# Performance work log

Hardware: AMD Instinct MI355X
Metric: run time of the kernel (lower is better)

## Reference

```python
import jax, jax.numpy as jnp
import numpy as np

NEG_SLOPE = 0.2  # PyG GATConv default negative_slope
EPS = 1e-16      # PyG softmax denominator eps


def gat_layer(x, src, dst, W, b, a_src, a_dst, n_nodes):
    # x: [N, Fin]; W: [Fout, Fin]; a_src/a_dst: [Fout] (heads=1, concat)
    h = x @ W.T                                   # [N, Fout]
    al_s = h @ a_src                              # [N]
    al_d = h @ a_dst                              # [N]
    e = jax.nn.leaky_relu(al_s[src] + al_d[dst], NEG_SLOPE)   # [E]
    m = jax.lax.stop_gradient(
        jax.ops.segment_max(e, dst, num_segments=n_nodes))   # stable softmax per target
    ex = jnp.exp(e - m[dst])
    denom = jax.ops.segment_sum(ex, dst, num_segments=n_nodes)
    alpha = ex / (denom[dst] + EPS)               # [E]
    out = jax.ops.segment_sum(alpha[:, None] * h[src], dst, num_segments=n_nodes)
    return out + b


def reference(x, edge_index, W0, b0, asrc0, adst0, W1, b1, asrc1, adst1):
    B, N, _ = x.shape
    # GATConv adds self-loops by default
    loops = jnp.arange(N, dtype=edge_index.dtype)
    src = jnp.concatenate([edge_index[0], loops])
    dst = jnp.concatenate([edge_index[1], loops])

    def per_graph(xb):
        h = jax.nn.relu(gat_layer(xb, src, dst, W0, b0, asrc0, adst0, N))
        h = jax.nn.relu(gat_layer(h, src, dst, W1, b1, asrc1, adst1, N))
        return h

    return jax.vmap(per_graph)(x)  # [B, N, Fout]


def setup_inputs() -> dict:
    key = jax.random.key(0)
    ks = jax.random.split(key, 10)
    B, N, E = 4, 10000, 320000
    F0, F1, F2 = 256, 256, 128
    x = jax.random.normal(ks[0], (B, N, F0), dtype=jnp.float32)
    edge_index = jax.random.randint(ks[1], (2, E), 0, N, dtype=jnp.int64)
    s0 = 1.0 / np.sqrt(F0)
    s1 = 1.0 / np.sqrt(F1)
    return {
        "x": x,
        "edge_index": edge_index,
        "W0": jax.random.normal(ks[2], (F1, F0), dtype=jnp.float32) * s0,
        "b0": jnp.zeros((F1,), dtype=jnp.float32),
        "asrc0": jax.random.normal(ks[3], (F1,), dtype=jnp.float32) * s1,
        "adst0": jax.random.normal(ks[4], (F1,), dtype=jnp.float32) * s1,
        "W1": jax.random.normal(ks[5], (F2, F1), dtype=jnp.float32) * s1,
        "b1": jnp.zeros((F2,), dtype=jnp.float32),
        "asrc1": jax.random.normal(ks[6], (F2,), dtype=jnp.float32) / np.sqrt(F2),
        "adst1": jax.random.normal(ks[7], (F2,), dtype=jnp.float32) / np.sqrt(F2),
    }
```

## Files before the change

kernel.cpp:

```cpp
#include <hip/hip_runtime.h>
#include <hip/hip_bf16.h>

#define NN 10000
#define EE 320000
#define BB 4
#define F0 256
#define F1 256
#define F2 128
#define ETOT (EE + NN)

typedef __attribute__((ext_vector_type(8))) short bf16x8;
typedef __attribute__((ext_vector_type(4))) float f32x4;

__device__ inline unsigned short f2bf_rn(float f) {
    unsigned int u = __float_as_uint(f);
    unsigned int r = (u + 0x7fffu + ((u >> 16) & 1u)) >> 16;
    return (unsigned short)r;
}
__device__ inline float bf2f(unsigned short s) {
    return __uint_as_float(((unsigned int)s) << 16);
}

__global__ void count_kernel(const int* __restrict__ ei, int* __restrict__ deg) {
    int id = blockIdx.x * blockDim.x + threadIdx.x;
    if (id >= ETOT) return;
    int dst = (id < EE) ? ei[EE + id] : (id - EE);
    atomicAdd(&deg[dst], 1);
}

__global__ void scan_kernel(const int* __restrict__ deg, int* __restrict__ rowstart) {
    __shared__ int part[256];
    int t = threadIdx.x;
    const int CH = (NN + 255) / 256;
    int lo = t * CH, hi = min(lo + CH, NN);
    int s = 0;
    for (int i = lo; i < hi; i++) s += deg[i];
    part[t] = s;
    __syncthreads();
    for (int off = 1; off < 256; off <<= 1) {
        int v = (t >= off) ? part[t - off] : 0;
        __syncthreads();
        part[t] += v;
        __syncthreads();
    }
    int run = (t == 0) ? 0 : part[t - 1];
    for (int i = lo; i < hi; i++) { int d = deg[i]; rowstart[i] = run; run += d; }
    if (t == 255) rowstart[NN] = run;
}

__global__ void scatter_kernel(const int* __restrict__ ei,
                               const int* __restrict__ rowstart,
                               int* __restrict__ fill,
                               int* __restrict__ sorted_src) {
    int id = blockIdx.x * blockDim.x + threadIdx.x;
    if (id >= ETOT) return;
    int src, dst;
    if (id < EE) { src = ei[id]; dst = ei[EE + id]; }
    else         { src = dst = id - EE; }
    int pos = rowstart[dst] + atomicAdd(&fill[dst], 1);
    sorted_src[pos] = src;
}

__global__ __launch_bounds__(256) void conv_split(const float* __restrict__ in,
                                                  unsigned short* __restrict__ out2,
                                                  int rows, int K) {
    int q = K >> 2;
    int id = blockIdx.x * blockDim.x + threadIdx.x;
    if (id >= rows * q) return;
    int r = id / q;
    int c4 = (id - r * q) << 2;
    float4 v = *(const float4*)(in + (size_t)r * K + c4);
    ushort4 hi, lo;
    hi.x = f2bf_rn(v.x); lo.x = f2bf_rn(v.x - bf2f(hi.x));
    hi.y = f2bf_rn(v.y); lo.y = f2bf_rn(v.y - bf2f(hi.y));
    hi.z = f2bf_rn(v.z); lo.z = f2bf_rn(v.z - bf2f(hi.z));
    hi.w = f2bf_rn(v.w); lo.w = f2bf_rn(v.w - bf2f(hi.w));
    unsigned short* o = out2 + (size_t)r * 2 * K;
    *(ushort4*)(o + c4) = hi;
    *(ushort4*)(o + K + c4) = lo;
}

template <int NT>
__global__ __launch_bounds__(256) void gemm_db(
    const unsigned short* __restrict__ A2,
    const unsigned short* __restrict__ B2,
    unsigned short* __restrict__ C,
    const float* __restrict__ asrc,
    const float* __restrict__ adst,
    float* __restrict__ als,
    float* __restrict__ ald,
    int M) {
    __shared__ unsigned short sbuf[20480];
    unsigned short* Ah = sbuf;
    unsigned short* Al = sbuf + 5120;
    unsigned short* Bh = sbuf + 10240;
    unsigned short* Bl = sbuf + 15360;

    int tid = threadIdx.x;
    int wave = tid >> 6, lane = tid & 63;
    int wm = wave & 1, wn = wave >> 1;
    int lq = lane >> 4, lm = lane & 15;
    int bm = blockIdx.x * 128;
    int bn = blockIdx.y * 128;

    f32x4 acc[4][4];
#pragma unroll
    for (int i = 0; i < 4; i++)
#pragma unroll
        for (int j = 0; j < 4; j++) {
            acc[i][j][0] = 0.f; acc[i][j][1] = 0.f;
            acc[i][j][2] = 0.f; acc[i][j][3] = 0.f;
        }

    int r0 = tid >> 2, sub = tid & 3;
    int ar0 = min(bm + r0, M - 1), ar1 = min(bm + r0 + 64, M - 1);
    const unsigned short* aSrc0 = A2 + (size_t)ar0 * 512 + sub * 8;
    const unsigned short* aSrc1 = A2 + (size_t)ar1 * 512 + sub * 8;
    const unsigned short* bSrc0 = B2 + (size_t)(bn + r0) * 512 + sub * 8;
    const unsigned short* bSrc1 = B2 + (size_t)(bn + r0 + 64) * 512 + sub * 8;
    int ld0 = r0 * 40 + sub * 8;
    int ld1 = (r0 + 64) * 40 + sub * 8;

    uint4 pAh0, pAh1, pAl0, pAl1, pBh0, pBh1, pBl0, pBl1;

    auto loadreg = [&](int c) {
        int o = c * 32;
        pAh0 = *(const uint4*)(aSrc0 + o);       pAh1 = *(const uint4*)(aSrc1 + o);
        pAl0 = *(const uint4*)(aSrc0 + 256 + o); pAl1 = *(const uint4*)(aSrc1 + 256 + o);
        pBh0 = *(const uint4*)(bSrc0 + o);       pBh1 = *(const uint4*)(bSrc1 + o);
        pBl0 = *(const uint4*)(bSrc0 + 256 + o); pBl1 = *(const uint4*)(bSrc1 + 256 + o);
    };
    auto writereg = [&]() {
        *(uint4*)(Ah + ld0) = pAh0; *(uint4*)(Ah + ld1) = pAh1;
        *(uint4*)(Al + ld0) = pAl0; *(uint4*)(Al + ld1) = pAl1;
        *(uint4*)(Bh + ld0) = pBh0; *(uint4*)(Bh + ld1) = pBh1;
        *(uint4*)(Bl + ld0) = pBl0; *(uint4*)(Bl + ld1) = pBl1;
    };

    loadreg(0);
#pragma unroll 1
    for (int c = 0; c < 8; c++) {
        __syncthreads();
        writereg();
        __syncthreads();
        if (c < 7) loadreg(c + 1);

        bf16x8 afh[4], afl[4];
#pragma unroll
        for (int i = 0; i < 4; i++) {
            int row = wm * 64 + i * 16 + lm;
            afh[i] = *(const bf16x8*)(Ah + row * 40 + lq * 8);
            afl[i] = *(const bf16x8*)(Al + row * 40 + lq * 8);
        }
#pragma unroll
        for (int j = 0; j < 4; j++) {
            int row = wn * 64 + j * 16 + lm;
            bf16x8 bh = *(const bf16x8*)(Bh + row * 40 + lq * 8);
            bf16x8 bl = *(const bf16x8*)(Bl + row * 40 + lq * 8);
#pragma unroll
            for (int i = 0; i < 4; i++) {
                acc[i][j] = __builtin_amdgcn_mfma_f32_16x16x32_bf16(afh[i], bh, acc[i][j], 0, 0, 0);
                acc[i][j] = __builtin_amdgcn_mfma_f32_16x16x32_bf16(afl[i], bh, acc[i][j], 0, 0, 0);
                acc[i][j] = __builtin_amdgcn_mfma_f32_16x16x32_bf16(afh[i], bl, acc[i][j], 0, 0, 0);
            }
        }
    }

    __syncthreads();

    unsigned short* Cs = sbuf;
#pragma unroll
    for (int i = 0; i < 4; i++) {
#pragma unroll
        for (int rr = 0; rr < 4; rr++) {
            int row = wm * 64 + i * 16 + lq * 4 + rr;
#pragma unroll
            for (int j = 0; j < 4; j++)
                Cs[row * 136 + wn * 64 + j * 16 + lm] = f2bf_rn(acc[i][j][rr]);
        }
    }
    __syncthreads();

    {
        int r = tid >> 1;
        int cl = (tid & 1) * 64;
        float s = 0.f, d = 0.f;
#pragma unroll
        for (int c8 = 0; c8 < 8; c8++) {
            bf16x8 v8 = *(const bf16x8*)(Cs + r * 136 + cl + c8 * 8);
#pragma unroll
            for (int u = 0; u < 8; u++) {
                float v = bf2f((unsigned short)v8[u]);
                s += v * asrc[bn + cl + c8 * 8 + u];
                d += v * adst[bn + cl + c8 * 8 + u];
            }
        }
        s += __shfl_xor(s, 1); d += __shfl_xor(d, 1);
        if ((tid & 1) == 0 && (bm + r) < M) {
            atomicAdd(&als[bm + r], s);
            atomicAdd(&ald[bm + r], d);
        }
    }

#pragma unroll
    for (int k = 0; k < 8; k++) {
        int u = k * 256 + tid;
        int row = u >> 4, q = u & 15;
        if (bm + row < M)
            *(uint4*)(C + (size_t)(bm + row) * NT + bn + q * 8) = *(const uint4*)(Cs + row * 136 + q * 8);
    }
}

template <int F, int OUTMODE>
__global__ __launch_bounds__(256) void agg_kernel(const unsigned short* __restrict__ h,
                                                  const float* __restrict__ als,
                                                  const float* __restrict__ ald,
                                                  const int* __restrict__ rowstart,
                                                  const int* __restrict__ sorted_src,
                                                  const float* __restrict__ bias,
                                                  float* __restrict__ out,
                                                  unsigned short* __restrict__ out2) {
    constexpr int V = F / 64;
    typedef unsigned short usv __attribute__((ext_vector_type(V)));
    typedef float fvec __attribute__((ext_vector_type(V)));

    int wid = (blockIdx.x * blockDim.x + threadIdx.x) >> 6;
    int lane = threadIdx.x & 63;
    int b = wid / NN;
    int n = wid - b * NN;

    const float* als_b = als + (size_t)b * NN;
    float aldn = ald[wid];
    int rs = rowstart[n];
    int deg = rowstart[n + 1] - rs;
    const unsigned short* hb = h + (size_t)b * NN * F;

    fvec acc;
#pragma unroll
    for (int u = 0; u < V; u++) acc[u] = 0.f;
    float sum = 0.f;

    for (int c0 = 0; c0 < deg; c0 += 64) {
        int j = c0 + lane;
        float ex = 0.f;
        int srcj = 0;
        if (j < deg) {
            srcj = sorted_src[rs + j];
            float e = als_b[srcj] + aldn;
            e = e > 0.f ? e : 0.2f * e;
            ex = __expf(e);
        }
        sum += ex;
        int cnt = min(64, deg - c0);

        int nfull = cnt >> 4;
        for (int g = 0; g < nfull; g++) {
            int bse = g << 4;
            int s[16]; float w[16];
#pragma unroll
            for (int i = 0; i < 16; i++) {
                s[i] = __shfl(srcj, bse + i);
                w[i] = __shfl(ex, bse + i);
            }
            usv r[16];
#pragma unroll
            for (int i = 0; i < 16; i++)
                r[i] = *(const usv*)(hb + (size_t)s[i] * F + lane * V);
#pragma unroll
            for (int i = 0; i < 16; i++)
#pragma unroll
                for (int u = 0; u < V; u++) acc[u] += w[i] * bf2f(r[i][u]);
        }
        for (int bse = nfull << 4; bse < cnt; bse += 4) {
            int s[4]; float w[4];
#pragma unroll
            for (int i = 0; i < 4; i++) {
                s[i] = __shfl(srcj, bse + i);
                w[i] = __shfl(ex, bse + i);
            }
            usv r[4];
#pragma unroll
            for (int i = 0; i < 4; i++)
                r[i] = *(const usv*)(hb + (size_t)s[i] * F + lane * V);
#pragma unroll
            for (int i = 0; i < 4; i++)
#pragma unroll
                for (int u = 0; u < V; u++) acc[u] += w[i] * bf2f(r[i][u]);
        }
    }
#pragma unroll
    for (int off = 32; off; off >>= 1) sum += __shfl_xor(sum, off);
    float inv = 1.0f / (sum + 1e-16f);

    fvec r;
#pragma unroll
    for (int u = 0; u < V; u++) {
        float v = acc[u] * inv + bias[lane * V + u];
        r[u] = fmaxf(v, 0.f);
    }
    if (OUTMODE == 0) {
        *(fvec*)(out + (size_t)wid * F + lane * V) = r;
    } else {
        ushort4 hi, lo;
        hi.x = f2bf_rn(r[0]); lo.x = f2bf_rn(r[0] - bf2f(hi.x));
        hi.y = f2bf_rn(r[1]); lo.y = f2bf_rn(r[1] - bf2f(hi.y));
        hi.z = f2bf_rn(r[2]); lo.z = f2bf_rn(r[2] - bf2f(hi.z));
        hi.w = f2bf_rn(r[3]); lo.w = f2bf_rn(r[3] - bf2f(hi.w));
        unsigned short* o = out2 + (size_t)wid * 2 * F;
        *(ushort4*)(o + lane * 4) = hi;
        *(ushort4*)(o + F + lane * 4) = lo;
    }
}

extern "C" void kernel_launch(void* const* d_in, const int* in_sizes, int n_in,
                              void* d_out, int out_size, void* d_ws, size_t ws_size,
                              hipStream_t stream) {
    const float* x     = (const float*)d_in[0];
    const int*   ei    = (const int*)d_in[1];
    const float* W0    = (const float*)d_in[2];
    const float* b0    = (const float*)d_in[3];
    const float* asrc0 = (const float*)d_in[4];
    const float* adst0 = (const float*)d_in[5];
    const float* W1    = (const float*)d_in[6];
    const float* b1    = (const float*)d_in[7];
    const float* asrc1 = (const float*)d_in[8];
    const float* adst1 = (const float*)d_in[9];
    float* outp = (float*)d_out;

    const int M = BB * NN;

    size_t off = 0;
    char* base = (char*)d_ws;
    auto alloc = [&](size_t bytes) {
        void* p = base + off;
        off += (bytes + 255) & ~(size_t)255;
        return p;
    };
    int*   deg        = (int*)alloc((size_t)NN * 4);
    int*   fill       = (int*)alloc((size_t)NN * 4);
    int*   rowstart   = (int*)alloc((size_t)(NN + 1) * 4);
    int*   sorted_src = (int*)alloc((size_t)ETOT * 4);
    unsigned short* A2  = (unsigned short*)alloc((size_t)M * 512 * 2);
    unsigned short* W02 = (unsigned short*)alloc((size_t)F1 * 512 * 2);
    unsigned short* W12 = (unsigned short*)alloc((size_t)F2 * 512 * 2);
    unsigned short* h   = (unsigned short*)alloc((size_t)M * F1 * 2);
    float* als        = (float*)alloc((size_t)M * 4);
    float* ald        = (float*)alloc((size_t)M * 4);

    hipMemsetAsync(deg, 0, (char*)fill - (char*)deg + (size_t)NN * 4, stream);

    int egrid = (ETOT + 255) / 256;
    count_kernel<<<egrid, 256, 0, stream>>>(ei, deg);
    scan_kernel<<<1, 256, 0, stream>>>(deg, rowstart);
    scatter_kernel<<<egrid, 256, 0, stream>>>(ei, rowstart, fill, sorted_src);

    int wgrid = (M * 64) / 256;

    conv_split<<<(M * (F0 / 4) + 255) / 256, 256, 0, stream>>>(x, A2, M, F0);
    conv_split<<<(F1 * (F0 / 4) + 255) / 256, 256, 0, stream>>>(W0, W02, F1, F0);
    conv_split<<<(F2 * (F1 / 4) + 255) / 256, 256, 0, stream>>>(W1, W12, F2, F1);

    int mtiles = (M + 127) / 128;

    hipMemsetAsync(als, 0, (size_t)2 * M * 4, stream);
    gemm_db<F1><<<dim3(mtiles, F1 / 128), 256, 0, stream>>>(A2, W02, h, asrc0, adst0, als, ald, M);
    agg_kernel<F1, 1><<<wgrid, 256, 0, stream>>>(h, als, ald, rowstart, sorted_src, b0,
                                                 nullptr, A2 );

    hipMemsetAsync(als, 0, (size_t)2 * M * 4, stream);
    gemm_db<F2><<<dim3(mtiles, F2 / 128), 256, 0, stream>>>(A2, W12, h, asrc1, adst1, als, ald, M);
    agg_kernel<F2, 0><<<wgrid, 256, 0, stream>>>(h, als, ald, rowstart, sorted_src, b1,
                                                 outp, nullptr);
}
```

Before: 322.9 us.

## Interleave batch into node-major layout and aggregate all graphs per node together

Converts the input to a node-major interleaved layout (row n*4+b), so the GEMM outputs h, als and ald come out with the four graphs of each node adjacent. The aggregation kernel now gives one wavefront per node: four 16-lane groups each handle one graph. Each edge's source index and its four als values are then read once and shared across all graphs, and the four h rows of a source sit contiguously in memory. This cuts repeated reads of sorted_src and the degree data, improves locality of the gathers, and writes the final output back in batch-major order. In exchange each lane holds more accumulators (FB floats), which may raise register pressure, and the unroll depth per neighbor batch drops from 16 to 4.

```diff
diff --git a/kernel.cpp b/kernel.cpp
--- a/kernel.cpp
+++ b/kernel.cpp
@@ -11,6 +11,7 @@
 
 typedef __attribute__((ext_vector_type(8))) short bf16x8;
 typedef __attribute__((ext_vector_type(4))) float f32x4;
+typedef unsigned short us8 __attribute__((ext_vector_type(8)));
 
 __device__ inline unsigned short f2bf_rn(float f) {
     unsigned int u = __float_as_uint(f);
@@ -61,6 +62,7 @@
     sorted_src[pos] = src;
 }
 
+template <int ILV>
 __global__ __launch_bounds__(256) void conv_split(const float* __restrict__ in,
                                                   unsigned short* __restrict__ out2,
                                                   int rows, int K) {
@@ -75,7 +77,12 @@
     hi.y = f2bf_rn(v.y); lo.y = f2bf_rn(v.y - bf2f(hi.y));
     hi.z = f2bf_rn(v.z); lo.z = f2bf_rn(v.z - bf2f(hi.z));
     hi.w = f2bf_rn(v.w); lo.w = f2bf_rn(v.w - bf2f(hi.w));
-    unsigned short* o = out2 + (size_t)r * 2 * K;
+    int ro = r;
+    if (ILV) {
+        int b = r / NN, n = r - b * NN;
+        ro = n * 4 + b;
+    }
+    unsigned short* o = out2 + (size_t)ro * 2 * K;
     *(ushort4*)(o + c4) = hi;
     *(ushort4*)(o + K + c4) = lo;
 }
@@ -212,103 +219,116 @@
 }
 
 template <int F, int OUTMODE>
-__global__ __launch_bounds__(256) void agg_kernel(const unsigned short* __restrict__ h,
-                                                  const float* __restrict__ als,
-                                                  const float* __restrict__ ald,
-                                                  const int* __restrict__ rowstart,
-                                                  const int* __restrict__ sorted_src,
-                                                  const float* __restrict__ bias,
-                                                  float* __restrict__ out,
-                                                  unsigned short* __restrict__ out2) {
-    constexpr int V = F / 64;
-    typedef unsigned short usv __attribute__((ext_vector_type(V)));
-    typedef float fvec __attribute__((ext_vector_type(V)));
-
-    int wid = (blockIdx.x * blockDim.x + threadIdx.x) >> 6;
+__global__ __launch_bounds__(256) void agg_batched(
+    const unsigned short* __restrict__ h,
+    const float* __restrict__ als,
+    const float* __restrict__ ald,
+    const int* __restrict__ rowstart,
+    const int* __restrict__ sorted_src,
+    const float* __restrict__ bias,
+    float* __restrict__ out,
+    unsigned short* __restrict__ out2) {
+    constexpr int FB = F / 16;
+    constexpr int NL = FB / 8;
+
+    int n = blockIdx.x * 4 + (threadIdx.x >> 6);
     int lane = threadIdx.x & 63;
-    int b = wid / NN;
-    int n = wid - b * NN;
-
-    const float* als_b = als + (size_t)b * NN;
-    float aldn = ald[wid];
+    int g = lane >> 4, fb = lane & 15;
+
+    float4 ald4 = *(const float4*)(ald + (size_t)n * 4);
     int rs = rowstart[n];
     int deg = rowstart[n + 1] - rs;
-    const unsigned short* hb = h + (size_t)b * NN * F;
-
-    fvec acc;
-#pragma unroll
-    for (int u = 0; u < V; u++) acc[u] = 0.f;
-    float sum = 0.f;
+
+    float acc[FB];
+#pragma unroll
+    for (int u = 0; u < FB; u++) acc[u] = 0.f;
+    float4 sum4 = make_float4(0.f, 0.f, 0.f, 0.f);
 
     for (int c0 = 0; c0 < deg; c0 += 64) {
         int j = c0 + lane;
-        float ex = 0.f;
+        float4 ex4 = make_float4(0.f, 0.f, 0.f, 0.f);
         int srcj = 0;
         if (j < deg) {
             srcj = sorted_src[rs + j];
-            float e = als_b[srcj] + aldn;
-            e = e > 0.f ? e : 0.2f * e;
-            ex = __expf(e);
-        }
-        sum += ex;
+            float4 a4 = *(const float4*)(als + (size_t)srcj * 4);
+            float e;
+            e = a4.x + ald4.x; e = e > 0.f ? e : 0.2f * e; ex4.x = __expf(e);
+            e = a4.y + ald4.y; e = e > 0.f ? e : 0.2f * e; ex4.y = __expf(e);
+            e = a4.z + ald4.z; e = e > 0.f ? e : 0.2f * e; ex4.z = __expf(e);
+            e = a4.w + ald4.w; e = e > 0.f ? e : 0.2f * e; ex4.w = __expf(e);
+        }
+        sum4.x += ex4.x; sum4.y += ex4.y; sum4.z += ex4.z; sum4.w += ex4.w;
+
         int cnt = min(64, deg - c0);
-
-        int nfull = cnt >> 4;
-        for (int g = 0; g < nfull; g++) {
-            int bse = g << 4;
-            int s[16]; float w[16];
-#pragma unroll
-            for (int i = 0; i < 16; i++) {
-                s[i] = __shfl(srcj, bse + i);
-                w[i] = __shfl(ex, bse + i);
-            }
-            usv r[16];
-#pragma unroll
-            for (int i = 0; i < 16; i++)
-                r[i] = *(const usv*)(hb + (size_t)s[i] * F + lane * V);
-#pragma unroll
-            for (int i = 0; i < 16; i++)
-#pragma unroll
-                for (int u = 0; u < V; u++) acc[u] += w[i] * bf2f(r[i][u]);
-        }
-        for (int bse = nfull << 4; bse < cnt; bse += 4) {
-            int s[4]; float w[4];
+        for (int bse = 0; bse < cnt; bse += 4) {
+            int sj[4]; float wsel[4];
 #pragma unroll
             for (int i = 0; i < 4; i++) {
-                s[i] = __shfl(srcj, bse + i);
-                w[i] = __shfl(ex, bse + i);
-            }
-            usv r[4];
+                sj[i] = __shfl(srcj, bse + i);
+                float w0 = __shfl(ex4.x, bse + i), w1 = __shfl(ex4.y, bse + i);
+                float w2 = __shfl(ex4.z, bse + i), w3 = __shfl(ex4.w, bse + i);
+                float wa = (g & 1) ? w1 : w0;
+                float wb = (g & 1) ? w3 : w2;
+                wsel[i] = (g & 2) ? wb : wa;
+            }
+            us8 r[4][NL];
+#pragma unroll
+            for (int i = 0; i < 4; i++) {
+                const unsigned short* p = h + ((size_t)sj[i] * 4 + g) * F + fb * FB;
+#pragma unroll
+                for (int l = 0; l < NL; l++) r[i][l] = *(const us8*)(p + l * 8);
+            }
 #pragma unroll
             for (int i = 0; i < 4; i++)
-                r[i] = *(const usv*)(hb + (size_t)s[i] * F + lane * V);
-#pragma unroll
-            for (int i = 0; i < 4; i++)
-#pragma unroll
-                for (int u = 0; u < V; u++) acc[u] += w[i] * bf2f(r[i][u]);
-        }
-    }
-#pragma unroll
-    for (int off = 32; off; off >>= 1) sum += __shfl_xor(sum, off);
-    float inv = 1.0f / (sum + 1e-16f);
-
-    fvec r;
-#pragma unroll
-    for (int u = 0; u < V; u++) {
-        float v = acc[u] * inv + bias[lane * V + u];
-        r[u] = fmaxf(v, 0.f);
-    }
+#pragma unroll
+                for (int l = 0; l < NL; l++)
+#pragma unroll
+                    for (int u = 0; u < 8; u++)
+                        acc[l * 8 + u] += wsel[i] * bf2f((unsigned short)r[i][l][u]);
+        }
+    }
+
+#pragma unroll
+    for (int off = 32; off; off >>= 1) {
+        sum4.x += __shfl_xor(sum4.x, off);
+        sum4.y += __shfl_xor(sum4.y, off);
+        sum4.z += __shfl_xor(sum4.z, off);
+        sum4.w += __shfl_xor(sum4.w, off);
+    }
+    float sa = (g & 1) ? sum4.y : sum4.x;
+    float sb = (g & 1) ? sum4.w : sum4.z;
+    float sg = (g & 2) ? sb : sa;
+    float inv = 1.0f / (sg + 1e-16f);
+
+    float rv[FB];
+#pragma unroll
+    for (int u = 0; u < FB; u++) {
+        float v = acc[u] * inv + bias[fb * FB + u];
+        rv[u] = fmaxf(v, 0.f);
+    }
+
     if (OUTMODE == 0) {
-        *(fvec*)(out + (size_t)wid * F + lane * V) = r;
+        float* o = out + ((size_t)g * NN + n) * F + fb * FB;
+#pragma unroll
+        for (int l = 0; l < FB / 4; l++)
+            *(float4*)(o + l * 4) = make_float4(rv[l * 4], rv[l * 4 + 1], rv[l * 4 + 2], rv[l * 4 + 3]);
     } else {
-        ushort4 hi, lo;
-        hi.x = f2bf_rn(r[0]); lo.x = f2bf_rn(r[0] - bf2f(hi.x));
-        hi.y = f2bf_rn(r[1]); lo.y = f2bf_rn(r[1] - bf2f(hi.y));
-        hi.z = f2bf_rn(r[2]); lo.z = f2bf_rn(r[2] - bf2f(hi.z));
-        hi.w = f2bf_rn(r[3]); lo.w = f2bf_rn(r[3] - bf2f(hi.w));
-        unsigned short* o = out2 + (size_t)wid * 2 * F;
-        *(ushort4*)(o + lane * 4) = hi;
-        *(ushort4*)(o + F + lane * 4) = lo;
+        us8 hi8[NL], lo8[NL];
+#pragma unroll
+        for (int l = 0; l < NL; l++)
+#pragma unroll
+            for (int u = 0; u < 8; u++) {
+                float v = rv[l * 8 + u];
+                unsigned short hv = f2bf_rn(v);
+                hi8[l][u] = hv;
+                lo8[l][u] = f2bf_rn(v - bf2f(hv));
+            }
+        unsigned short* o = out2 + ((size_t)n * 4 + g) * 2 * F + fb * FB;
+#pragma unroll
+        for (int l = 0; l < NL; l++) {
+            *(us8*)(o + l * 8) = hi8[l];
+            *(us8*)(o + F + l * 8) = lo8[l];
+        }
     }
 }
 
@@ -354,21 +374,20 @@
     scan_kernel<<<1, 256, 0, stream>>>(deg, rowstart);
     scatter_kernel<<<egrid, 256, 0, stream>>>(ei, rowstart, fill, sorted_src);
 
-    int wgrid = (M * 64) / 256;
-
-    conv_split<<<(M * (F0 / 4) + 255) / 256, 256, 0, stream>>>(x, A2, M, F0);
-    conv_split<<<(F1 * (F0 / 4) + 255) / 256, 256, 0, stream>>>(W0, W02, F1, F0);
-    conv_split<<<(F2 * (F1 / 4) + 255) / 256, 256, 0, stream>>>(W1, W12, F2, F1);
+    conv_split<1><<<(M * (F0 / 4) + 255) / 256, 256, 0, stream>>>(x, A2, M, F0);
+    conv_split<0><<<(F1 * (F0 / 4) + 255) / 256, 256, 0, stream>>>(W0, W02, F1, F0);
+    conv_split<0><<<(F2 * (F1 / 4) + 255) / 256, 256, 0, stream>>>(W1, W12, F2, F1);
 
     int mtiles = (M + 127) / 128;
+    int agrid = NN / 4;
 
     hipMemsetAsync(als, 0, (size_t)2 * M * 4, stream);
     gemm_db<F1><<<dim3(mtiles, F1 / 128), 256, 0, stream>>>(A2, W02, h, asrc0, adst0, als, ald, M);
-    agg_kernel<F1, 1><<<wgrid, 256, 0, stream>>>(h, als, ald, rowstart, sorted_src, b0,
-                                                 nullptr, A2 );
+    agg_batched<F1, 1><<<agrid, 256, 0, stream>>>(h, als, ald, rowstart, sorted_src, b0,
+                                                  nullptr, A2 );
 
     hipMemsetAsync(als, 0, (size_t)2 * M * 4, stream);
     gemm_db<F2><<<dim3(mtiles, F2 / 128), 256, 0, stream>>>(A2, W12, h, asrc1, adst1, als, ald, M);
-    agg_kernel<F2, 0><<<wgrid, 256, 0, stream>>>(h, als, ald, rowstart, sorted_src, b1,
-                                                 outp, nullptr);
-}
+    agg_batched<F2, 0><<<agrid, 256, 0, stream>>>(h, als, ald, rowstart, sorted_src, b1,
+                                                  outp, nullptr);
+}
```

Measured after the change: 343.0 us. 1.06x slower.

## Fuse fp32 input split into GEMM, shrink M tile, drop attention atomics

Applied to the files above, without the earlier changes.

The first GEMM now reads fp32 x directly and does the hi/lo bf16 split while staging to shared memory, which removes the separate conversion kernel and its round trip through global memory. The M tile drops from 128 to 64, giving 625 row blocks for better occupancy on the small N dimension. Per-column-block attention partials go to a 2-wide buffer with plain stores instead of atomics, so the memsets are no longer needed, and agg sums the two halves. The two weight conversions are merged into one launch. The trade-off is extra conversion ALU inside the GEMM and more B-tile reloads because of the smaller M tile.

```diff
diff --git a/kernel.cpp b/kernel.cpp
--- a/kernel.cpp
+++ b/kernel.cpp
@@ -11,6 +11,7 @@
 
 typedef __attribute__((ext_vector_type(8))) short bf16x8;
 typedef __attribute__((ext_vector_type(4))) float f32x4;
+typedef unsigned short us8 __attribute__((ext_vector_type(8)));
 
 __device__ inline unsigned short f2bf_rn(float f) {
     unsigned int u = __float_as_uint(f);
@@ -61,51 +62,54 @@
     sorted_src[pos] = src;
 }
 
-__global__ __launch_bounds__(256) void conv_split(const float* __restrict__ in,
-                                                  unsigned short* __restrict__ out2,
-                                                  int rows, int K) {
-    int q = K >> 2;
-    int id = blockIdx.x * blockDim.x + threadIdx.x;
-    if (id >= rows * q) return;
-    int r = id / q;
-    int c4 = (id - r * q) << 2;
-    float4 v = *(const float4*)(in + (size_t)r * K + c4);
+__global__ __launch_bounds__(256) void conv_split_w(const float* __restrict__ W0,
+                                                    const float* __restrict__ W1,
+                                                    unsigned short* __restrict__ W02,
+                                                    unsigned short* __restrict__ W12) {
+    int id = blockIdx.x * 256 + threadIdx.x;
+    if (id >= (F1 + F2) * 64) return;
+    int r = id >> 6, c4 = (id & 63) << 2;
+    const float* src;
+    unsigned short* dst;
+    if (r < F1) { src = W0 + (size_t)r * 256;        dst = W02 + (size_t)r * 512; }
+    else        { src = W1 + (size_t)(r - F1) * 256; dst = W12 + (size_t)(r - F1) * 512; }
+    float4 v = *(const float4*)(src + c4);
     ushort4 hi, lo;
     hi.x = f2bf_rn(v.x); lo.x = f2bf_rn(v.x - bf2f(hi.x));
     hi.y = f2bf_rn(v.y); lo.y = f2bf_rn(v.y - bf2f(hi.y));
     hi.z = f2bf_rn(v.z); lo.z = f2bf_rn(v.z - bf2f(hi.z));
     hi.w = f2bf_rn(v.w); lo.w = f2bf_rn(v.w - bf2f(hi.w));
-    unsigned short* o = out2 + (size_t)r * 2 * K;
-    *(ushort4*)(o + c4) = hi;
-    *(ushort4*)(o + K + c4) = lo;
-}
-
-template <int NT>
+    *(ushort4*)(dst + c4) = hi;
+    *(ushort4*)(dst + 256 + c4) = lo;
+}
+
+template <int NT, int XF32>
 __global__ __launch_bounds__(256) void gemm_db(
+    const float* __restrict__ Af,
     const unsigned short* __restrict__ A2,
     const unsigned short* __restrict__ B2,
     unsigned short* __restrict__ C,
     const float* __restrict__ asrc,
     const float* __restrict__ adst,
-    float* __restrict__ als,
-    float* __restrict__ ald,
-    int M) {
-    __shared__ unsigned short sbuf[20480];
+    float* __restrict__ als2,
+    float* __restrict__ ald2) {
+    __shared__ unsigned short sbuf[15360];
     unsigned short* Ah = sbuf;
-    unsigned short* Al = sbuf + 5120;
-    unsigned short* Bh = sbuf + 10240;
-    unsigned short* Bl = sbuf + 15360;
+    unsigned short* Al = sbuf + 2560;
+    unsigned short* Bh = sbuf + 5120;
+    unsigned short* Bl = sbuf + 10240;
 
     int tid = threadIdx.x;
     int wave = tid >> 6, lane = tid & 63;
     int wm = wave & 1, wn = wave >> 1;
     int lq = lane >> 4, lm = lane & 15;
-    int bm = blockIdx.x * 128;
-    int bn = blockIdx.y * 128;
-
-    f32x4 acc[4][4];
-#pragma unroll
-    for (int i = 0; i < 4; i++)
+    int bm = blockIdx.x * 64;
+    int by = blockIdx.y;
+    int bn = by * 128;
+
+    f32x4 acc[2][4];
+#pragma unroll
+    for (int i = 0; i < 2; i++)
 #pragma unroll
         for (int j = 0; j < 4; j++) {
             acc[i][j][0] = 0.f; acc[i][j][1] = 0.f;
@@ -113,28 +117,48 @@
         }
 
     int r0 = tid >> 2, sub = tid & 3;
-    int ar0 = min(bm + r0, M - 1), ar1 = min(bm + r0 + 64, M - 1);
-    const unsigned short* aSrc0 = A2 + (size_t)ar0 * 512 + sub * 8;
-    const unsigned short* aSrc1 = A2 + (size_t)ar1 * 512 + sub * 8;
+    const unsigned short* aSrc2 = A2 + (size_t)(bm + r0) * 512 + sub * 8;
+    const float* aSrcF = Af + (size_t)(bm + r0) * 256 + sub * 8;
     const unsigned short* bSrc0 = B2 + (size_t)(bn + r0) * 512 + sub * 8;
     const unsigned short* bSrc1 = B2 + (size_t)(bn + r0 + 64) * 512 + sub * 8;
-    int ld0 = r0 * 40 + sub * 8;
-    int ld1 = (r0 + 64) * 40 + sub * 8;
-
-    uint4 pAh0, pAh1, pAl0, pAl1, pBh0, pBh1, pBl0, pBl1;
+    int lda = r0 * 40 + sub * 8;
+    int ldb0 = r0 * 40 + sub * 8;
+    int ldb1 = (r0 + 64) * 40 + sub * 8;
+
+    uint4 pAh, pAl, pBh0, pBh1, pBl0, pBl1;
+    float4 pF0, pF1;
 
     auto loadreg = [&](int c) {
         int o = c * 32;
-        pAh0 = *(const uint4*)(aSrc0 + o);       pAh1 = *(const uint4*)(aSrc1 + o);
-        pAl0 = *(const uint4*)(aSrc0 + 256 + o); pAl1 = *(const uint4*)(aSrc1 + 256 + o);
+        if (XF32) {
+            pF0 = *(const float4*)(aSrcF + o);
+            pF1 = *(const float4*)(aSrcF + o + 4);
+        } else {
+            pAh = *(const uint4*)(aSrc2 + o);
+            pAl = *(const uint4*)(aSrc2 + 256 + o);
+        }
         pBh0 = *(const uint4*)(bSrc0 + o);       pBh1 = *(const uint4*)(bSrc1 + o);
         pBl0 = *(const uint4*)(bSrc0 + 256 + o); pBl1 = *(const uint4*)(bSrc1 + 256 + o);
     };
     auto writereg = [&]() {
-        *(uint4*)(Ah + ld0) = pAh0; *(uint4*)(Ah + ld1) = pAh1;
-        *(uint4*)(Al + ld0) = pAl0; *(uint4*)(Al + ld1) = pAl1;
-        *(uint4*)(Bh + ld0) = pBh0; *(uint4*)(Bh + ld1) = pBh1;
-        *(uint4*)(Bl + ld0) = pBl0; *(uint4*)(Bl + ld1) = pBl1;
+        if (XF32) {
+            float fa[8];
+            *(float4*)&fa[0] = pF0; *(float4*)&fa[4] = pF1;
+            us8 hs, ls;
+#pragma unroll
+            for (int u = 0; u < 8; u++) {
+                unsigned short hv = f2bf_rn(fa[u]);
+                hs[u] = hv;
+                ls[u] = f2bf_rn(fa[u] - bf2f(hv));
+            }
+            *(us8*)(Ah + lda) = hs;
+            *(us8*)(Al + lda) = ls;
+        } else {
+            *(uint4*)(Ah + lda) = pAh;
+            *(uint4*)(Al + lda) = pAl;
+        }
+        *(uint4*)(Bh + ldb0) = pBh0; *(uint4*)(Bh + ldb1) = pBh1;
+        *(uint4*)(Bl + ldb0) = pBl0; *(uint4*)(Bl + ldb1) = pBl1;
     };
 
     loadreg(0);
@@ -145,10 +169,10 @@
         __syncthreads();
         if (c < 7) loadreg(c + 1);
 
-        bf16x8 afh[4], afl[4];
-#pragma unroll
-        for (int i = 0; i < 4; i++) {
-            int row = wm * 64 + i * 16 + lm;
+        bf16x8 afh[2], afl[2];
+#pragma unroll
+        for (int i = 0; i < 2; i++) {
+            int row = wm * 32 + i * 16 + lm;
             afh[i] = *(const bf16x8*)(Ah + row * 40 + lq * 8);
             afl[i] = *(const bf16x8*)(Al + row * 40 + lq * 8);
         }
@@ -158,7 +182,7 @@
             bf16x8 bh = *(const bf16x8*)(Bh + row * 40 + lq * 8);
             bf16x8 bl = *(const bf16x8*)(Bl + row * 40 + lq * 8);
 #pragma unroll
-            for (int i = 0; i < 4; i++) {
+            for (int i = 0; i < 2; i++) {
                 acc[i][j] = __builtin_amdgcn_mfma_f32_16x16x32_bf16(afh[i], bh, acc[i][j], 0, 0, 0);
                 acc[i][j] = __builtin_amdgcn_mfma_f32_16x16x32_bf16(afl[i], bh, acc[i][j], 0, 0, 0);
                 acc[i][j] = __builtin_amdgcn_mfma_f32_16x16x32_bf16(afh[i], bl, acc[i][j], 0, 0, 0);
@@ -170,10 +194,10 @@
 
     unsigned short* Cs = sbuf;
 #pragma unroll
-    for (int i = 0; i < 4; i++) {
+    for (int i = 0; i < 2; i++) {
 #pragma unroll
         for (int rr = 0; rr < 4; rr++) {
-            int row = wm * 64 + i * 16 + lq * 4 + rr;
+            int row = wm * 32 + i * 16 + lq * 4 + rr;
 #pragma unroll
             for (int j = 0; j < 4; j++)
                 Cs[row * 136 + wn * 64 + j * 16 + lm] = f2bf_rn(acc[i][j][rr]);
@@ -182,39 +206,43 @@
     __syncthreads();
 
     {
-        int r = tid >> 1;
-        int cl = (tid & 1) * 64;
+        int r = tid >> 2;
+        int cseg = (tid & 3) * 32;
         float s = 0.f, d = 0.f;
 #pragma unroll
-        for (int c8 = 0; c8 < 8; c8++) {
-            bf16x8 v8 = *(const bf16x8*)(Cs + r * 136 + cl + c8 * 8);
+        for (int c8 = 0; c8 < 4; c8++) {
+            bf16x8 v8 = *(const bf16x8*)(Cs + r * 136 + cseg + c8 * 8);
 #pragma unroll
             for (int u = 0; u < 8; u++) {
                 float v = bf2f((unsigned short)v8[u]);
-                s += v * asrc[bn + cl + c8 * 8 + u];
-                d += v * adst[bn + cl + c8 * 8 + u];
+                s += v * asrc[bn + cseg + c8 * 8 + u];
+                d += v * adst[bn + cseg + c8 * 8 + u];
             }
         }
         s += __shfl_xor(s, 1); d += __shfl_xor(d, 1);
-        if ((tid & 1) == 0 && (bm + r) < M) {
-            atomicAdd(&als[bm + r], s);
-            atomicAdd(&ald[bm + r], d);
-        }
-    }
-
-#pragma unroll
-    for (int k = 0; k < 8; k++) {
+        s += __shfl_xor(s, 2); d += __shfl_xor(d, 2);
+        if ((tid & 3) == 0) {
+            als2[(size_t)(bm + r) * 2 + by] = s;
+            ald2[(size_t)(bm + r) * 2 + by] = d;
+        }
+        if (NT == 128 && (tid & 3) == 1) {
+            als2[(size_t)(bm + r) * 2 + 1] = 0.f;
+            ald2[(size_t)(bm + r) * 2 + 1] = 0.f;
+        }
+    }
+
+#pragma unroll
+    for (int k = 0; k < 4; k++) {
         int u = k * 256 + tid;
         int row = u >> 4, q = u & 15;
-        if (bm + row < M)
-            *(uint4*)(C + (size_t)(bm + row) * NT + bn + q * 8) = *(const uint4*)(Cs + row * 136 + q * 8);
+        *(uint4*)(C + (size_t)(bm + row) * NT + bn + q * 8) = *(const uint4*)(Cs + row * 136 + q * 8);
     }
 }
 
 template <int F, int OUTMODE>
 __global__ __launch_bounds__(256) void agg_kernel(const unsigned short* __restrict__ h,
-                                                  const float* __restrict__ als,
-                                                  const float* __restrict__ ald,
+                                                  const float* __restrict__ als2,
+                                                  const float* __restrict__ ald2,
                                                   const int* __restrict__ rowstart,
                                                   const int* __restrict__ sorted_src,
                                                   const float* __restrict__ bias,
@@ -229,8 +257,9 @@
     int b = wid / NN;
     int n = wid - b * NN;
 
-    const float* als_b = als + (size_t)b * NN;
-    float aldn = ald[wid];
+    const float2* als_b = (const float2*)als2 + (size_t)b * NN;
+    float2 d2 = ((const float2*)ald2)[wid];
+    float aldn = d2.x + d2.y;
     int rs = rowstart[n];
     int deg = rowstart[n + 1] - rs;
     const unsigned short* hb = h + (size_t)b * NN * F;
@@ -246,7 +275,8 @@
         int srcj = 0;
         if (j < deg) {
             srcj = sorted_src[rs + j];
-            float e = als_b[srcj] + aldn;
+            float2 a2 = als_b[srcj];
+            float e = a2.x + a2.y + aldn;
             e = e > 0.f ? e : 0.2f * e;
             ex = __expf(e);
         }
@@ -344,8 +374,8 @@
     unsigned short* W02 = (unsigned short*)alloc((size_t)F1 * 512 * 2);
     unsigned short* W12 = (unsigned short*)alloc((size_t)F2 * 512 * 2);
     unsigned short* h   = (unsigned short*)alloc((size_t)M * F1 * 2);
-    float* als        = (float*)alloc((size_t)M * 4);
-    float* ald        = (float*)alloc((size_t)M * 4);
+    float* als2       = (float*)alloc((size_t)M * 2 * 4);
+    float* ald2       = (float*)alloc((size_t)M * 2 * 4);
 
     hipMemsetAsync(deg, 0, (char*)fill - (char*)deg + (size_t)NN * 4, stream);
 
@@ -354,21 +384,17 @@
     scan_kernel<<<1, 256, 0, stream>>>(deg, rowstart);
     scatter_kernel<<<egrid, 256, 0, stream>>>(ei, rowstart, fill, sorted_src);
 
+    conv_split_w<<<((F1 + F2) * 64 + 255) / 256, 256, 0, stream>>>(W0, W1, W02, W12);
+
     int wgrid = (M * 64) / 256;
 
-    conv_split<<<(M * (F0 / 4) + 255) / 256, 256, 0, stream>>>(x, A2, M, F0);
-    conv_split<<<(F1 * (F0 / 4) + 255) / 256, 256, 0, stream>>>(W0, W02, F1, F0);
-    conv_split<<<(F2 * (F1 / 4) + 255) / 256, 256, 0, stream>>>(W1, W12, F2, F1);
-
-    int mtiles = (M + 127) / 128;
-
-    hipMemsetAsync(als, 0, (size_t)2 * M * 4, stream);
-    gemm_db<F1><<<dim3(mtiles, F1 / 128), 256, 0, stream>>>(A2, W02, h, asrc0, adst0, als, ald, M);
-    agg_kernel<F1, 1><<<wgrid, 256, 0, stream>>>(h, als, ald, rowstart, sorted_src, b0,
+    gemm_db<F1, 1><<<dim3(625, F1 / 128), 256, 0, stream>>>(x, nullptr, W02, h,
+                                                            asrc0, adst0, als2, ald2);
+    agg_kernel<F1, 1><<<wgrid, 256, 0, stream>>>(h, als2, ald2, rowstart, sorted_src, b0,
                                                  nullptr, A2 );
 
-    hipMemsetAsync(als, 0, (size_t)2 * M * 4, stream);
-    gemm_db<F2><<<dim3(mtiles, F2 / 128), 256, 0, stream>>>(A2, W12, h, asrc1, adst1, als, ald, M);
-    agg_kernel<F2, 0><<<wgrid, 256, 0, stream>>>(h, als, ald, rowstart, sorted_src, b1,
+    gemm_db<F2, 0><<<dim3(625, F2 / 128), 256, 0, stream>>>(nullptr, A2, W12, h,
+                                                            asrc1, adst1, als2, ald2);
+    agg_kernel<F2, 0><<<wgrid, 256, 0, stream>>>(h, als2, ald2, rowstart, sorted_src, b1,
                                                  outp, nullptr);
 }
```

Result: faster. 311.0 us (-3.7%).
